# Optimization experiments

Hardware: AMD Instinct MI355X
Metric: run time of the kernel (lower is better)

Reference implementation:

```python
import jax, jax.numpy as jnp
import numpy as np

B, C, H, W = 8, 256, 128, 128
NUM_S, MIDS, K = 64, 8, 8  # plane_mid, mids, node_num
HW = H * W
EPS = 1e-9


def _pool_mat(n, o):
    # adaptive avg pool 1D as a (o, n) averaging matrix (torch AdaptiveAvgPool2d bins)
    M = np.zeros((o, n), np.float32)
    for i in range(o):
        s = (i * n) // o
        e = -((-(i + 1) * n) // o)  # ceil((i+1)*n/o)
        M[i, s:e] = 1.0 / (e - s)
    return jnp.asarray(M)


def setup_inputs() -> dict:
    key = jax.random.key(0)
    ks = jax.random.split(key, 11)
    rn = lambda k, shp, s=1.0: jax.random.normal(k, shp, jnp.float32) * s
    return {
        "x": rn(ks[0], (B, C, H, W)),
        "contour": rn(ks[1], (B, 2, H, W)),
        "conv_state_w": rn(ks[2], (NUM_S, C), 0.06),
        "conv_state_b": jnp.zeros((NUM_S,), jnp.float32),
        "conv_proj_w": rn(ks[3], (NUM_S, C), 0.06),
        "conv_proj_b": jnp.zeros((NUM_S,), jnp.float32),
        "anchor": jax.random.uniform(ks[4], (K, C), jnp.float32),
        "sigma_p": jax.random.uniform(ks[5], (K, C), jnp.float32),
        "gcn_w1": rn(ks[6], (C, C), 0.06),
        "gcn_w2": rn(ks[7], (C, C), 0.06),
        "gcn_w3": rn(ks[8], (C, C), 0.06),
    }


def reference(x, contour, conv_state_w, conv_state_b, conv_proj_w, conv_proj_b,
              anchor, sigma_p, gcn_w1, gcn_w2, gcn_w3):
    b, c, h, w = x.shape
    hw = h * w
    xf = x.reshape(b, c, hw)                                       # (B,C,HW)

    # ---- EnhanceModule: contour-masked projection -> anchors -> softmax assignment ----
    # contour already at x's spatial size, so F.interpolate is identity
    cm = jax.nn.softmax(contour, axis=1)[:, 1:2]                    # (B,1,H,W)
    x_proj = jnp.einsum('sc,bcn->bsn', conv_proj_w, xf) + conv_proj_b[None, :, None]  # (B,S,HW)
    x_mask = x_proj.reshape(b, NUM_S, h, w) * cm                    # (B,S,H,W)
    Mh, Mw = _pool_mat(h, MIDS + 2), _pool_mat(w, MIDS + 2)
    pooled = jnp.einsum('oh,bshw,pw->bsop', Mh, x_mask, Mw)         # adaptive avg pool (B,S,10,10)
    x_anchor = pooled[:, :, 1:-1, 1:-1].reshape(b, NUM_S, MIDS * MIDS)  # (B,S,mids^2)
    proj = jnp.einsum('bsm,bsn->bmn', x_anchor, x_proj)             # (B,mids^2,HW)
    proj = jax.nn.softmax(proj, axis=1)

    # ---- GraphNet (NetVLAD-style), vectorized over nodes ----
    sigma = jax.nn.sigmoid(sigma_p)                                 # (K,C)
    inv2 = 1.0 / (sigma * sigma)
    xn = xf.transpose(0, 2, 1)                                      # (B,HW,C)
    # ||(x_n - a_k)/sigma_k||^2 via quadratic expansion (no (B,K,HW,C) tensor)
    d2 = (jnp.einsum('bnc,kc->bkn', xn * xn, inv2)
          - 2.0 * jnp.einsum('bnc,kc->bkn', xn, anchor * inv2)
          + jnp.sum(anchor * anchor * inv2, axis=1)[None, :, None])  # (B,K,HW)
    soft = jax.nn.softmax(-0.5 * d2, axis=1)                        # (B,K,HW)
    ssum = soft.sum(-1)                                             # (B,K)
    wsum = jnp.einsum('bkn,bnc->bkc', soft, xn)                     # (B,K,C)
    nodes = (wsum - anchor[None] * ssum[..., None]) / sigma[None] / (ssum[..., None] + EPS)
    nodes = nodes / jnp.maximum(jnp.linalg.norm(nodes, axis=2, keepdims=True), 1e-12)
    flat = nodes.reshape(b, -1)
    flat = flat / jnp.maximum(jnp.linalg.norm(flat, axis=1, keepdims=True), 1e-12)
    g = flat.reshape(b, c, K)  # torch .view reinterpret (NOT transpose)

    # ---- CascadeGCNet, loop=3 ----
    for Wg in (gcn_w1, gcn_w2, gcn_w3):
        gt = g.transpose(0, 2, 1)                                   # (B,K,C)
        adj = jax.nn.softmax(jnp.einsum('bkc,bcj->bkj', gt, g), axis=2)  # (B,K,K)
        support = jnp.einsum('bkc,cd->bkd', gt, Wg)                 # (B,K,C)
        g = jnp.einsum('bkj,bjd->bdk', adj, support)                # (B,C,K)
    g = jax.nn.relu(g)
    return (g, proj, soft)
```

## Files before the change

### kernel.cpp

```cpp
#include <hip/hip_runtime.h>
#include <math.h>

#define HW 16384
#define B_ 8
#define C_ 256
#define S_ 64
#define K_ 8

__device__ __forceinline__ float sigmoidf_(float z) { return 1.f / (1.f + __expf(-z)); }

__global__ __launch_bounds__(256) void k0_prep(const float* __restrict__ anchor,
                                               const float* __restrict__ sigma_p,
                                               const float* __restrict__ wproj,
                                               unsigned short* __restrict__ Wtb,
                                               float* __restrict__ iva2,
                                               float* __restrict__ kconst, float* __restrict__ ssumg) {
    const int c = threadIdx.x;
    const int lane = c & 63, wid = c >> 6;
    __shared__ float red[4][8];
    float kc[8];
#pragma unroll
    for (int k = 0; k < 8; ++k) {
        float sg = sigmoidf_(sigma_p[k * C_ + c]);
        float iv = 1.f / (sg * sg);
        float a = anchor[k * C_ + c];
        const int r = k >> 1, j = k & 1;
        iva2[c * 16 + r * 4 + j] = a * iv;
        iva2[c * 16 + r * 4 + 2 + j] = iv;
        kc[k] = a * a * iv;
    }
    for (int s = 0; s < S_; ++s) {
        unsigned u = __float_as_uint(wproj[s * C_ + c]);
        unsigned r16 = (u + 0x7fffu + ((u >> 16) & 1u)) >> 16;
        Wtb[c * S_ + s] = (unsigned short)r16;
    }
    if (c < 64) ssumg[c] = 0.f;
#pragma unroll
    for (int m = 32; m; m >>= 1) {
#pragma unroll
        for (int k = 0; k < 8; ++k) kc[k] += __shfl_xor(kc[k], m, 64);
    }
    if (lane == 0) {
#pragma unroll
        for (int k = 0; k < 8; ++k) red[wid][k] = kc[k];
    }
    __syncthreads();
    if (c < 8) kconst[c] = red[0][c] + red[1][c] + red[2][c] + red[3][c];
}

__global__ __launch_bounds__(256) void k1_fused(
    const float* __restrict__ x, const float* __restrict__ contour,
    const unsigned short* __restrict__ Wtb, const float* __restrict__ bproj,
    const float* __restrict__ iva2, const float* __restrict__ kconst,
    float* __restrict__ cm, float* __restrict__ xp, float* __restrict__ soft,
    float* __restrict__ ssumg) {
    __shared__ unsigned short Wl[C_ * S_];
    __shared__ float xl[2][8][256];
    __shared__ float Ql[C_ * 16];
    const int tid = threadIdx.x;
    const int lane = tid & 63;
    const int r = __builtin_amdgcn_readfirstlane(tid >> 6);
    const int s0 = r * 16;
    const int b = blockIdx.y;
    const int pl = lane * 4;
    const int px = blockIdx.x * 256 + pl;

    const float* xb = x + (size_t)b * C_ * HW + px;

    {
        const uint4* src = (const uint4*)Wtb;
        uint4* dst = (uint4*)Wl;
        for (int i = tid; i < C_ * S_ / 8; i += 256) dst[i] = src[i];
        const float4* qs = (const float4*)iva2;
        float4* qd = (float4*)Ql;
        for (int i = tid; i < C_ * 16 / 4; i += 256) qd[i] = qs[i];
        *(float4*)&xl[0][r][pl] = *(const float4*)(xb + (size_t)r * HW);
        *(float4*)&xl[0][4 + r][pl] = *(const float4*)(xb + (size_t)(4 + r) * HW);
    }
    __syncthreads();

    float4 acc[16];
#pragma unroll
    for (int s = 0; s < 16; ++s) acc[s] = make_float4(0.f, 0.f, 0.f, 0.f);
    float4 q1a = make_float4(0.f, 0.f, 0.f, 0.f), q1b = q1a, q2a = q1a, q2b = q1a;

    int buf = 0;
    for (int ch = 0; ch < C_; ch += 8) {
        const bool more = (ch + 8) < C_;
        float4 nv0, nv1;
        if (more) {
            nv0 = *(const float4*)(xb + (size_t)(ch + 8 + r) * HW);
            nv1 = *(const float4*)(xb + (size_t)(ch + 12 + r) * HW);
        }
#pragma unroll
        for (int j = 0; j < 8; ++j) {
            const int c = ch + j;
            const float4 xv = *(const float4*)&xl[buf][j][pl];
            const unsigned short* wr = Wl + (size_t)c * S_ + s0;
            const uint4 wA = *(const uint4*)wr;
            const uint4 wB = *(const uint4*)(wr + 8);
            const unsigned pw[8] = {wA.x, wA.y, wA.z, wA.w, wB.x, wB.y, wB.z, wB.w};
#pragma unroll
            for (int p = 0; p < 8; ++p) {
                const float wlo = __uint_as_float(pw[p] << 16);
                const float whi = __uint_as_float(pw[p] & 0xffff0000u);
                float4& aL = acc[2 * p];
                float4& aH = acc[2 * p + 1];
                aL.x = fmaf(wlo, xv.x, aL.x); aL.y = fmaf(wlo, xv.y, aL.y);
                aL.z = fmaf(wlo, xv.z, aL.z); aL.w = fmaf(wlo, xv.w, aL.w);
                aH.x = fmaf(whi, xv.x, aH.x); aH.y = fmaf(whi, xv.y, aH.y);
                aH.z = fmaf(whi, xv.z, aH.z); aH.w = fmaf(whi, xv.w, aH.w);
            }
            const float4 t = *(const float4*)&Ql[c * 16 + r * 4];
            float4 x2;
            x2.x = xv.x * xv.x; x2.y = xv.y * xv.y; x2.z = xv.z * xv.z; x2.w = xv.w * xv.w;
            q1a.x = fmaf(t.x, xv.x, q1a.x); q1a.y = fmaf(t.x, xv.y, q1a.y);
            q1a.z = fmaf(t.x, xv.z, q1a.z); q1a.w = fmaf(t.x, xv.w, q1a.w);
            q1b.x = fmaf(t.y, xv.x, q1b.x); q1b.y = fmaf(t.y, xv.y, q1b.y);
            q1b.z = fmaf(t.y, xv.z, q1b.z); q1b.w = fmaf(t.y, xv.w, q1b.w);
            q2a.x = fmaf(t.z, x2.x, q2a.x); q2a.y = fmaf(t.z, x2.y, q2a.y);
            q2a.z = fmaf(t.z, x2.z, q2a.z); q2a.w = fmaf(t.z, x2.w, q2a.w);
            q2b.x = fmaf(t.w, x2.x, q2b.x); q2b.y = fmaf(t.w, x2.y, q2b.y);
            q2b.z = fmaf(t.w, x2.z, q2b.z); q2b.w = fmaf(t.w, x2.w, q2b.w);
        }
        if (more) {
            *(float4*)&xl[buf ^ 1][r][pl] = nv0;
            *(float4*)&xl[buf ^ 1][4 + r][pl] = nv1;
        }
        __syncthreads();
        buf ^= 1;
    }

#pragma unroll
    for (int s = 0; s < 16; ++s) {
        const float bias = bproj[s0 + s];
        float4 o;
        o.x = acc[s].x + bias; o.y = acc[s].y + bias;
        o.z = acc[s].z + bias; o.w = acc[s].w + bias;
        *(float4*)(xp + ((size_t)b * S_ + s0 + s) * HW + px) = o;
    }

    float* qb = (float*)xl;
    *(float4*)&qb[(2 * r) * 256 + pl] = q1a;
    *(float4*)&qb[(2 * r + 1) * 256 + pl] = q1b;
    *(float4*)&qb[2048 + (2 * r) * 256 + pl] = q2a;
    *(float4*)&qb[2048 + (2 * r + 1) * 256 + pl] = q2b;
    __syncthreads();

    if (r == 0) {
        float4 lgv[K_];
        float4 mx = make_float4(-1e30f, -1e30f, -1e30f, -1e30f);
#pragma unroll
        for (int k = 0; k < K_; ++k) {
            const float4 q1k = *(const float4*)&qb[k * 256 + pl];
            const float4 q2k = *(const float4*)&qb[2048 + k * 256 + pl];
            const float kc = kconst[k];
            lgv[k].x = -0.5f * (q2k.x - 2.f * q1k.x + kc);
            lgv[k].y = -0.5f * (q2k.y - 2.f * q1k.y + kc);
            lgv[k].z = -0.5f * (q2k.z - 2.f * q1k.z + kc);
            lgv[k].w = -0.5f * (q2k.w - 2.f * q1k.w + kc);
            mx.x = fmaxf(mx.x, lgv[k].x); mx.y = fmaxf(mx.y, lgv[k].y);
            mx.z = fmaxf(mx.z, lgv[k].z); mx.w = fmaxf(mx.w, lgv[k].w);
        }
        float4 sm = make_float4(0.f, 0.f, 0.f, 0.f);
#pragma unroll
        for (int k = 0; k < K_; ++k) {
            lgv[k].x = __expf(lgv[k].x - mx.x); sm.x += lgv[k].x;
            lgv[k].y = __expf(lgv[k].y - mx.y); sm.y += lgv[k].y;
            lgv[k].z = __expf(lgv[k].z - mx.z); sm.z += lgv[k].z;
            lgv[k].w = __expf(lgv[k].w - mx.w); sm.w += lgv[k].w;
        }
        const float ix = 1.f / sm.x, iy = 1.f / sm.y, iz = 1.f / sm.z, iw = 1.f / sm.w;
        float ssk[K_];
#pragma unroll
        for (int k = 0; k < K_; ++k) {
            float4 o;
            o.x = lgv[k].x * ix; o.y = lgv[k].y * iy;
            o.z = lgv[k].z * iz; o.w = lgv[k].w * iw;
            *(float4*)(soft + ((size_t)b * K_ + k) * HW + px) = o;
            ssk[k] = (o.x + o.y) + (o.z + o.w);
        }
#pragma unroll
        for (int m = 32; m; m >>= 1) {
#pragma unroll
            for (int k = 0; k < K_; ++k) ssk[k] += __shfl_xor(ssk[k], m, 64);
        }
        if (lane == 0) {
#pragma unroll
            for (int k = 0; k < K_; ++k) atomicAdd(ssumg + b * 8 + k, ssk[k]);
        }

        const float4 c0 = *(const float4*)(contour + (size_t)b * 2 * HW + px);
        const float4 c1 = *(const float4*)(contour + (size_t)b * 2 * HW + HW + px);
        float4 cv;
        cv.x = sigmoidf_(c1.x - c0.x); cv.y = sigmoidf_(c1.y - c0.y);
        cv.z = sigmoidf_(c1.z - c0.z); cv.w = sigmoidf_(c1.w - c0.w);
        *(float4*)(cm + (size_t)b * HW + px) = cv;
    }
}

__global__ void k2_anchor(const float* __restrict__ xp, const float* __restrict__ cm,
                          float* __restrict__ xa) {
    __shared__ float col[128];
    const int i = blockIdx.x;
    const int s = blockIdx.y;
    const int b = blockIdx.z;
    const int w = threadIdx.x;
    const int h0 = ((i + 1) * 128) / 10;
    const int h1 = ((i + 2) * 128 + 9) / 10;
    const float* xps = xp + ((size_t)b * S_ + s) * HW;
    const float* cmb = cm + (size_t)b * HW;
    float v = 0.f;
    for (int h = h0; h < h1; ++h) v += xps[h * 128 + w] * cmb[h * 128 + w];
    col[w] = v;
    __syncthreads();
    if (w < 8) {
        const int j = w;
        const int w0 = ((j + 1) * 128) / 10;
        const int w1 = ((j + 2) * 128 + 9) / 10;
        float sum = 0.f;
        for (int t = w0; t < w1; ++t) sum += col[t];
        xa[((size_t)b * S_ + s) * 64 + i * 8 + j] = sum / (float)((h1 - h0) * (w1 - w0));
    }
}

__global__ __launch_bounds__(256, 4) void k3_proj(const float* __restrict__ xa,
                                                  float* __restrict__ xp) {
    const int tid = threadIdx.x;
    const int lane = tid & 63;
    const int wid = __builtin_amdgcn_readfirstlane(tid >> 6);
    const int pg = wid & 1;
    const int sh = wid >> 1;
    const int b = blockIdx.y;
    const int n = blockIdx.x * 128 + pg * 64 + lane;
    const float* xab = xa + (size_t)b * 4096;

    float p[64];
#pragma unroll
    for (int m = 0; m < 64; ++m) p[m] = 0.f;

    float* xpb = xp + (size_t)b * S_ * HW + n;
    const int s0 = sh * 32;
    float xv = xpb[(size_t)s0 * HW];
    for (int si = 0; si < 32; ++si) {
        const int s = s0 + si;
        float xnext = (si < 31) ? xpb[(size_t)(s + 1) * HW] : 0.f;
        const float* row = xab + s * 64;
#pragma unroll
        for (int m = 0; m < 64; ++m) p[m] = fmaf(row[m], xv, p[m]);
        xv = xnext;
    }

    __shared__ float lds[2][64][64];
    if (sh) {
#pragma unroll
        for (int m = 0; m < 64; ++m) lds[pg][m][lane] = p[m];
    }
    __syncthreads();
    if (!sh) {
#pragma unroll
        for (int m = 0; m < 64; ++m) p[m] += lds[pg][m][lane];
        float mx = -1e30f;
#pragma unroll
        for (int m = 0; m < 64; ++m) mx = fmaxf(mx, p[m]);
        float sm = 0.f;
#pragma unroll
        for (int m = 0; m < 64; ++m) { float e = __expf(p[m] - mx); p[m] = e; sm += e; }
        const float inv = 1.f / sm;
#pragma unroll
        for (int m = 0; m < 64; ++m) xpb[(size_t)m * HW] = p[m] * inv;
    }
}

__global__ __launch_bounds__(256) void k5_wsum(const float* __restrict__ x,
                                               const float* __restrict__ soft,
                                               float* __restrict__ wsum) {
    const int b = blockIdx.y;
    const int c0 = blockIdx.x * 2;
    const int tid = threadIdx.x;
    float a[16];
#pragma unroll
    for (int i = 0; i < 16; ++i) a[i] = 0.f;
    const float4* sb = (const float4*)(soft + (size_t)b * K_ * HW);
    const float4* xb = (const float4*)(x + ((size_t)b * C_ + c0) * HW);
    for (int i = tid; i < HW / 4; i += 256) {
        float4 sv[8];
#pragma unroll
        for (int k = 0; k < 8; ++k) sv[k] = sb[(size_t)k * (HW / 4) + i];
#pragma unroll
        for (int ci = 0; ci < 2; ++ci) {
            float4 xv = xb[(size_t)ci * (HW / 4) + i];
#pragma unroll
            for (int k = 0; k < 8; ++k) {
                float t = fmaf(sv[k].x, xv.x, fmaf(sv[k].y, xv.y,
                          fmaf(sv[k].z, xv.z, sv[k].w * xv.w)));
                a[ci * 8 + k] += t;
            }
        }
    }
    __shared__ float red[64];
    const int lane = tid & 63, wid = tid >> 6;
#pragma unroll
    for (int o = 0; o < 16; ++o) {
        float v = a[o];
#pragma unroll
        for (int m = 32; m; m >>= 1) v += __shfl_xor(v, m, 64);
        if (lane == 0) red[wid * 16 + o] = v;
    }
    __syncthreads();
    if (tid < 16) {
        float r = red[tid] + red[16 + tid] + red[32 + tid] + red[48 + tid];
        int ci = tid >> 3, k = tid & 7;
        wsum[((size_t)b * K_ + k) * C_ + c0 + ci] = r;
    }
}

__device__ __forceinline__ float blockSum256(float v, volatile float* sc) {
#pragma unroll
    for (int m = 32; m; m >>= 1) v += __shfl_xor(v, m, 64);
    const int wid = threadIdx.x >> 6, lane = threadIdx.x & 63;
    __syncthreads();
    if (lane == 0) sc[wid] = v;
    __syncthreads();
    return sc[0] + sc[1] + sc[2] + sc[3];
}

__global__ __launch_bounds__(256) void k6_gcn(const float* __restrict__ ssumg,
                                              const float* __restrict__ wsum,
                                              const float* __restrict__ anchor,
                                              const float* __restrict__ sigma_p,
                                              const float* __restrict__ w1,
                                              const float* __restrict__ w2,
                                              const float* __restrict__ w3,
                                              float* __restrict__ gout) {
    const int b = blockIdx.x;
    const int tid = threadIdx.x;
    const int lane = tid & 63, wid = tid >> 6;
    __shared__ float g_lds[2048];
    __shared__ float A[64];
    __shared__ float sc[4];
    __shared__ float red8[4][8];
    __shared__ float ssk_s[8];

    if (tid < 8) ssk_s[tid] = ssumg[b * 8 + tid];
    __syncthreads();
    float ssk[8];
#pragma unroll
    for (int k = 0; k < 8; ++k) ssk[k] = ssk_s[k];

    const int c = tid;
    float node[8];
#pragma unroll
    for (int k = 0; k < 8; ++k) {
        float sg = sigmoidf_(sigma_p[k * C_ + c]);
        float w = wsum[((size_t)b * K_ + k) * C_ + c];
        node[k] = (w - anchor[k * C_ + c] * ssk[k]) / sg / (ssk[k] + 1e-9f);
    }
    float rn[8];
#pragma unroll
    for (int k = 0; k < 8; ++k) rn[k] = node[k] * node[k];
#pragma unroll
    for (int m = 32; m; m >>= 1) {
#pragma unroll
        for (int k = 0; k < 8; ++k) rn[k] += __shfl_xor(rn[k], m, 64);
    }
    if (lane == 0) {
#pragma unroll
        for (int k = 0; k < 8; ++k) red8[wid][k] = rn[k];
    }
    __syncthreads();
#pragma unroll
    for (int k = 0; k < 8; ++k) {
        float t = red8[0][k] + red8[1][k] + red8[2][k] + red8[3][k];
        node[k] /= fmaxf(sqrtf(t), 1e-12f);
    }
    float fs = 0.f;
#pragma unroll
    for (int k = 0; k < 8; ++k) fs += node[k] * node[k];
    float fn = blockSum256(fs, sc);
    float finv = 1.f / fmaxf(sqrtf(fn), 1e-12f);
#pragma unroll
    for (int k = 0; k < 8; ++k) g_lds[tid * 8 + k] = node[k] * finv;
    __syncthreads();

    const float* Ws[3] = {w1, w2, w3};
    for (int L = 0; L < 3; ++L) {
        {
            const int pair = tid >> 2, part = tid & 3;
            const int p = pair >> 3, q = pair & 7;
            float s = 0.f;
            for (int i = part * 64; i < part * 64 + 64; ++i)
                s += g_lds[i * 8 + p] * g_lds[i * 8 + q];
            s += __shfl_xor(s, 1, 64);
            s += __shfl_xor(s, 2, 64);
            if (part == 0) A[pair] = s;
        }
        __syncthreads();
        if (tid < 8) {
            float mx = -1e30f;
            for (int j = 0; j < 8; ++j) mx = fmaxf(mx, A[tid * 8 + j]);
            float sm = 0.f;
            for (int j = 0; j < 8; ++j) { float e = __expf(A[tid * 8 + j] - mx); A[tid * 8 + j] = e; sm += e; }
            float iv = 1.f / sm;
            for (int j = 0; j < 8; ++j) A[tid * 8 + j] *= iv;
        }
        __syncthreads();
        float sup[8];
#pragma unroll
        for (int j = 0; j < 8; ++j) sup[j] = 0.f;
        const float* W = Ws[L];
        float wv[8], wn[8];
#pragma unroll
        for (int i = 0; i < 8; ++i) wv[i] = W[(size_t)i * 256 + tid];
        for (int c0 = 0; c0 < 256; c0 += 8) {
            if (c0 + 8 < 256) {
#pragma unroll
                for (int i = 0; i < 8; ++i) wn[i] = W[(size_t)(c0 + 8 + i) * 256 + tid];
            }
#pragma unroll
            for (int i = 0; i < 8; ++i) {
#pragma unroll
                for (int j = 0; j < 8; ++j)
                    sup[j] = fmaf(g_lds[(c0 + i) * 8 + j], wv[i], sup[j]);
            }
#pragma unroll
            for (int i = 0; i < 8; ++i) wv[i] = wn[i];
        }
        float gn[8];
#pragma unroll
        for (int k = 0; k < 8; ++k) {
            float s = 0.f;
#pragma unroll
            for (int j = 0; j < 8; ++j) s += A[k * 8 + j] * sup[j];
            gn[k] = s;
        }
        __syncthreads();
#pragma unroll
        for (int k = 0; k < 8; ++k) g_lds[tid * 8 + k] = gn[k];
        __syncthreads();
    }
#pragma unroll
    for (int k = 0; k < 8; ++k)
        gout[(size_t)b * 2048 + tid * 8 + k] = fmaxf(g_lds[tid * 8 + k], 0.f);
}

extern "C" void kernel_launch(void* const* d_in, const int* in_sizes, int n_in,
                              void* d_out, int out_size, void* d_ws, size_t ws_size,
                              hipStream_t stream) {
    const float* x = (const float*)d_in[0];
    const float* contour = (const float*)d_in[1];
    const float* wproj = (const float*)d_in[4];
    const float* bproj = (const float*)d_in[5];
    const float* anchor = (const float*)d_in[6];
    const float* sigma_p = (const float*)d_in[7];
    const float* w1 = (const float*)d_in[8];
    const float* w2 = (const float*)d_in[9];
    const float* w3 = (const float*)d_in[10];

    float* out = (float*)d_out;
    float* g_out = out;
    float* xp = out + 16384;
    float* soft = out + 16384 + 8388608;

    float* ws = (float*)d_ws;
    float* cm = ws;
    float* xa = ws + 131072;
    float* wsum = ws + 163840;
    float* kconst = ws + 180224;
    float* ssumg = ws + 180232;
    float* iva2 = ws + 180296;
    unsigned short* Wtb = (unsigned short*)(ws + 184392);

    k0_prep<<<1, 256, 0, stream>>>(anchor, sigma_p, wproj, Wtb, iva2, kconst, ssumg);
    k1_fused<<<dim3(HW / 256, B_), 256, 0, stream>>>(x, contour, Wtb, bproj, iva2, kconst,
                                                     cm, xp, soft, ssumg);
    k2_anchor<<<dim3(8, 64, B_), 128, 0, stream>>>(xp, cm, xa);
    k3_proj<<<dim3(HW / 128, B_), 256, 0, stream>>>(xa, xp);
    k5_wsum<<<dim3(128, B_), 256, 0, stream>>>(x, soft, wsum);
    k6_gcn<<<B_, 256, 0, stream>>>(ssumg, wsum, anchor, sigma_p, w1, w2, w3, g_out);
}
```

Before: 232.8 us.

## Use direct global-to-LDS loads in k1 and split GCN into per-layer kernels

The projection kernel now stages x tiles with global_load_lds directly into shared memory instead of loading through registers and storing, freeing registers and instructions in the inner loop. The GCN stage is split into a node-normalisation kernel and three per-layer kernels that read g from global memory, also changing the node layout written to match a flat reinterpret. This adds extra kernel launches and global round trips for the small GCN part, and relies on correct completion ordering of the async LDS loads.

```diff
diff --git a/kernel.cpp b/kernel.cpp
--- a/kernel.cpp
+++ b/kernel.cpp
@@ -8,6 +8,12 @@
 #define K_ 8
 
 __device__ __forceinline__ float sigmoidf_(float z) { return 1.f / (1.f + __expf(-z)); }
+
+__device__ __forceinline__ void gl_lds16(const float* g, float* l) {
+    __builtin_amdgcn_global_load_lds(
+        (const __attribute__((address_space(1))) void*)(g),
+        (__attribute__((address_space(3))) void*)(l), 16, 0, 0);
+}
 
 __global__ __launch_bounds__(256) void k0_prep(const float* __restrict__ anchor,
                                                const float* __restrict__ sigma_p,
@@ -74,8 +80,8 @@
         const float4* qs = (const float4*)iva2;
         float4* qd = (float4*)Ql;
         for (int i = tid; i < C_ * 16 / 4; i += 256) qd[i] = qs[i];
-        *(float4*)&xl[0][r][pl] = *(const float4*)(xb + (size_t)r * HW);
-        *(float4*)&xl[0][4 + r][pl] = *(const float4*)(xb + (size_t)(4 + r) * HW);
+        gl_lds16(xb + (size_t)r * HW, &xl[0][r][0]);
+        gl_lds16(xb + (size_t)(4 + r) * HW, &xl[0][4 + r][0]);
     }
     __syncthreads();
 
@@ -87,10 +93,9 @@
     int buf = 0;
     for (int ch = 0; ch < C_; ch += 8) {
         const bool more = (ch + 8) < C_;
-        float4 nv0, nv1;
         if (more) {
-            nv0 = *(const float4*)(xb + (size_t)(ch + 8 + r) * HW);
-            nv1 = *(const float4*)(xb + (size_t)(ch + 12 + r) * HW);
+            gl_lds16(xb + (size_t)(ch + 8 + r) * HW, &xl[buf ^ 1][r][0]);
+            gl_lds16(xb + (size_t)(ch + 12 + r) * HW, &xl[buf ^ 1][4 + r][0]);
         }
 #pragma unroll
         for (int j = 0; j < 8; ++j) {
@@ -123,10 +128,6 @@
             q2b.x = fmaf(t.w, x2.x, q2b.x); q2b.y = fmaf(t.w, x2.y, q2b.y);
             q2b.z = fmaf(t.w, x2.z, q2b.z); q2b.w = fmaf(t.w, x2.w, q2b.w);
         }
-        if (more) {
-            *(float4*)&xl[buf ^ 1][r][pl] = nv0;
-            *(float4*)&xl[buf ^ 1][4 + r][pl] = nv1;
-        }
         __syncthreads();
         buf ^= 1;
     }
@@ -325,19 +326,14 @@
     return sc[0] + sc[1] + sc[2] + sc[3];
 }
 
-__global__ __launch_bounds__(256) void k6_gcn(const float* __restrict__ ssumg,
-                                              const float* __restrict__ wsum,
-                                              const float* __restrict__ anchor,
-                                              const float* __restrict__ sigma_p,
-                                              const float* __restrict__ w1,
-                                              const float* __restrict__ w2,
-                                              const float* __restrict__ w3,
-                                              float* __restrict__ gout) {
+__global__ __launch_bounds__(256) void k6a_nodes(const float* __restrict__ ssumg,
+                                                 const float* __restrict__ wsum,
+                                                 const float* __restrict__ anchor,
+                                                 const float* __restrict__ sigma_p,
+                                                 float* __restrict__ gA) {
     const int b = blockIdx.x;
     const int tid = threadIdx.x;
     const int lane = tid & 63, wid = tid >> 6;
-    __shared__ float g_lds[2048];
-    __shared__ float A[64];
     __shared__ float sc[4];
     __shared__ float red8[4][8];
     __shared__ float ssk_s[8];
@@ -380,68 +376,63 @@
     float fn = blockSum256(fs, sc);
     float finv = 1.f / fmaxf(sqrtf(fn), 1e-12f);
 #pragma unroll
-    for (int k = 0; k < 8; ++k) g_lds[tid * 8 + k] = node[k] * finv;
-    __syncthreads();
-
-    const float* Ws[3] = {w1, w2, w3};
-    for (int L = 0; L < 3; ++L) {
-        {
-            const int pair = tid >> 2, part = tid & 3;
-            const int p = pair >> 3, q = pair & 7;
-            float s = 0.f;
-            for (int i = part * 64; i < part * 64 + 64; ++i)
-                s += g_lds[i * 8 + p] * g_lds[i * 8 + q];
-            s += __shfl_xor(s, 1, 64);
-            s += __shfl_xor(s, 2, 64);
-            if (part == 0) A[pair] = s;
-        }
-        __syncthreads();
-        if (tid < 8) {
-            float mx = -1e30f;
-            for (int j = 0; j < 8; ++j) mx = fmaxf(mx, A[tid * 8 + j]);
-            float sm = 0.f;
-            for (int j = 0; j < 8; ++j) { float e = __expf(A[tid * 8 + j] - mx); A[tid * 8 + j] = e; sm += e; }
-            float iv = 1.f / sm;
-            for (int j = 0; j < 8; ++j) A[tid * 8 + j] *= iv;
-        }
-        __syncthreads();
-        float sup[8];
-#pragma unroll
-        for (int j = 0; j < 8; ++j) sup[j] = 0.f;
-        const float* W = Ws[L];
-        float wv[8], wn[8];
-#pragma unroll
-        for (int i = 0; i < 8; ++i) wv[i] = W[(size_t)i * 256 + tid];
-        for (int c0 = 0; c0 < 256; c0 += 8) {
-            if (c0 + 8 < 256) {
-#pragma unroll
-                for (int i = 0; i < 8; ++i) wn[i] = W[(size_t)(c0 + 8 + i) * 256 + tid];
-            }
-#pragma unroll
-            for (int i = 0; i < 8; ++i) {
-#pragma unroll
-                for (int j = 0; j < 8; ++j)
-                    sup[j] = fmaf(g_lds[(c0 + i) * 8 + j], wv[i], sup[j]);
-            }
-#pragma unroll
-            for (int i = 0; i < 8; ++i) wv[i] = wn[i];
-        }
-        float gn[8];
-#pragma unroll
-        for (int k = 0; k < 8; ++k) {
-            float s = 0.f;
-#pragma unroll
-            for (int j = 0; j < 8; ++j) s += A[k * 8 + j] * sup[j];
-            gn[k] = s;
-        }
-        __syncthreads();
-#pragma unroll
-        for (int k = 0; k < 8; ++k) g_lds[tid * 8 + k] = gn[k];
-        __syncthreads();
-    }
-#pragma unroll
-    for (int k = 0; k < 8; ++k)
-        gout[(size_t)b * 2048 + tid * 8 + k] = fmaxf(g_lds[tid * 8 + k], 0.f);
+    for (int k = 0; k < 8; ++k) gA[(size_t)b * 2048 + k * 256 + c] = node[k] * finv;
+}
+
+__global__ __launch_bounds__(256) void k6_layer(const float* __restrict__ gIn,
+                                                const float* __restrict__ W,
+                                                float* __restrict__ gOut, int relu) {
+    const int b = blockIdx.x;
+    const int tid = threadIdx.x;
+    __shared__ float gl[2048];
+    __shared__ float A[64];
+    const float* gb = gIn + (size_t)b * 2048;
+    for (int i = tid; i < 2048; i += 256) gl[i] = gb[i];
+    __syncthreads();
+    {
+        const int pair = tid >> 2, part = tid & 3;
+        const int p = pair >> 3, q = pair & 7;
+        float s = 0.f;
+        for (int i = part * 64; i < part * 64 + 64; ++i)
+            s += gl[i * 8 + p] * gl[i * 8 + q];
+        s += __shfl_xor(s, 1, 64);
+        s += __shfl_xor(s, 2, 64);
+        if (part == 0) A[pair] = s;
+    }
+    __syncthreads();
+    if (tid < 8) {
+        float mx = -1e30f;
+        for (int j = 0; j < 8; ++j) mx = fmaxf(mx, A[tid * 8 + j]);
+        float sm = 0.f;
+        for (int j = 0; j < 8; ++j) { float e = __expf(A[tid * 8 + j] - mx); A[tid * 8 + j] = e; sm += e; }
+        float iv = 1.f / sm;
+        for (int j = 0; j < 8; ++j) A[tid * 8 + j] *= iv;
+    }
+    __syncthreads();
+    const int d = tid;
+    float sup[8];
+#pragma unroll
+    for (int j = 0; j < 8; ++j) sup[j] = 0.f;
+#pragma unroll 4
+    for (int c = 0; c < 256; ++c) {
+        const float wv = W[(size_t)c * 256 + d];
+        const float* gr = gb + c * 8;
+#pragma unroll
+        for (int j = 0; j < 8; ++j) sup[j] = fmaf(gr[j], wv, sup[j]);
+    }
+    float gn[8];
+#pragma unroll
+    for (int k = 0; k < 8; ++k) {
+        float s = 0.f;
+#pragma unroll
+        for (int j = 0; j < 8; ++j) s += A[k * 8 + j] * sup[j];
+        gn[k] = relu ? fmaxf(s, 0.f) : s;
+    }
+    float4 o0, o1;
+    o0.x = gn[0]; o0.y = gn[1]; o0.z = gn[2]; o0.w = gn[3];
+    o1.x = gn[4]; o1.y = gn[5]; o1.z = gn[6]; o1.w = gn[7];
+    *(float4*)&gOut[(size_t)b * 2048 + d * 8] = o0;
+    *(float4*)&gOut[(size_t)b * 2048 + d * 8 + 4] = o1;
 }
 
 extern "C" void kernel_launch(void* const* d_in, const int* in_sizes, int n_in,
@@ -470,6 +461,8 @@
     float* ssumg = ws + 180232;
     float* iva2 = ws + 180296;
     unsigned short* Wtb = (unsigned short*)(ws + 184392);
+    float* gA = ws;
+    float* gB = ws + 16384;
 
     k0_prep<<<1, 256, 0, stream>>>(anchor, sigma_p, wproj, Wtb, iva2, kconst, ssumg);
     k1_fused<<<dim3(HW / 256, B_), 256, 0, stream>>>(x, contour, Wtb, bproj, iva2, kconst,
@@ -477,5 +470,8 @@
     k2_anchor<<<dim3(8, 64, B_), 128, 0, stream>>>(xp, cm, xa);
     k3_proj<<<dim3(HW / 128, B_), 256, 0, stream>>>(xa, xp);
     k5_wsum<<<dim3(128, B_), 256, 0, stream>>>(x, soft, wsum);
-    k6_gcn<<<B_, 256, 0, stream>>>(ssumg, wsum, anchor, sigma_p, w1, w2, w3, g_out);
-}
+    k6a_nodes<<<B_, 256, 0, stream>>>(ssumg, wsum, anchor, sigma_p, gA);
+    k6_layer<<<B_, 256, 0, stream>>>(gA, w1, gB, 0);
+    k6_layer<<<B_, 256, 0, stream>>>(gB, w2, gA, 0);
+    k6_layer<<<B_, 256, 0, stream>>>(gA, w3, g_out, 1);
+}
```

After: 309.2 us. 1.33x slower.
